# Kernel optimization log

Measured on AMD Instinct MI355X. Metric: run time of the kernel, lower is better.

The kernel has to match this reference:

```python
import jax, jax.numpy as jnp
import numpy as np

N_POINTS = 8192
N_DIM = 2
N_PAIRS = 262144


def setup_inputs() -> dict:
    key = jax.random.key(0)
    k1, k2, k3, k4 = jax.random.split(key, 4)
    logits = jax.random.normal(k1, (N_POINTS, N_DIM), dtype=jnp.float32)
    i = jax.random.randint(k2, (N_PAIRS,), 0, N_POINTS, dtype=jnp.int64)
    j = jax.random.randint(k3, (N_PAIRS,), 0, N_POINTS, dtype=jnp.int64)
    pij = jax.random.uniform(k4, (N_PAIRS,), dtype=jnp.float32, minval=1e-6, maxval=1.0)
    pij = pij / jnp.sum(pij)  # joint probabilities, strictly positive
    return {"pij": pij, "i": i, "j": j, "logits": logits}


def reference(pij, i, j, logits):
    # Pairwise squared distances via the norm expansion (same math as the
    # N x N x D expanded-subtract in the torch original, without the huge tensor).
    sq = jnp.sum(logits * logits, axis=1)                      # [N]
    dkl2 = sq[:, None] + sq[None, :] - 2.0 * (logits @ logits.T)  # [N, N]
    n_diag = logits.shape[0]
    # Student-t partition function, excluding the diagonal (each diag term is 1).
    part = jnp.sum(1.0 / (1.0 + dkl2)) - n_diag
    xi = logits[i]                                              # [E, D]
    xj = logits[j]                                              # [E, D]
    # NOTE: torch adds 1.0 elementwise BEFORE summing over D, so this is
    # (D + ||xi-xj||^2)^-1 — reproduced faithfully.
    num = 1.0 / jnp.sum(1.0 + (xi - xj) ** 2, axis=1)           # [E]
    qij = num / part
    return jnp.sum(pij * (jnp.log(pij) - jnp.log(qij)))
```

## Files before the change

### kernel.cpp

```cpp
#include <hip/hip_runtime.h>
#include <math.h>

#define N_POINTS 8192
#define N_PAIRS  262144

constexpr int BLOCKS  = 512;
constexpr int THREADS = 256;
constexpr int ROWS    = N_POINTS / BLOCKS;
constexpr int TPR     = THREADS / ROWS;
constexpr int EPB     = N_PAIRS / BLOCKS;

__global__ __launch_bounds__(THREADS)
void fused_kernel(const float* __restrict__ logits,
                  const float* __restrict__ pij,
                  const int* __restrict__ ei,
                  const int* __restrict__ ej,
                  float* __restrict__ partials) {
    __shared__ float2 pts[N_POINTS];
    __shared__ float wred[3][THREADS / 64];

    const int t = threadIdx.x;
    const int b = blockIdx.x;

    {
        const float4* src = (const float4*)logits;
        float4* dst = (float4*)pts;
        #pragma unroll
        for (int k = t; k < N_POINTS / 2; k += THREADS) dst[k] = src[k];
    }
    __syncthreads();

    const int row = b * ROWS + (t / TPR);
    const int c0  = t % TPR;
    const float px = pts[row].x;
    const float py = pts[row].y;

    float a0 = 0.f, a1 = 0.f, a2 = 0.f, a3 = 0.f;
    #pragma unroll 2
    for (int k = c0; k < N_POINTS; k += 4 * TPR) {
        const float2 p0 = pts[k];
        const float2 p1 = pts[k + TPR];
        const float2 p2 = pts[k + 2 * TPR];
        const float2 p3 = pts[k + 3 * TPR];
        float dx, dy, d2;
        dx = px - p0.x; dy = py - p0.y;
        d2 = __builtin_fmaf(dx, dx, __builtin_fmaf(dy, dy, 1.0f));
        a0 += __builtin_amdgcn_rcpf(d2);
        dx = px - p1.x; dy = py - p1.y;
        d2 = __builtin_fmaf(dx, dx, __builtin_fmaf(dy, dy, 1.0f));
        a1 += __builtin_amdgcn_rcpf(d2);
        dx = px - p2.x; dy = py - p2.y;
        d2 = __builtin_fmaf(dx, dx, __builtin_fmaf(dy, dy, 1.0f));
        a2 += __builtin_amdgcn_rcpf(d2);
        dx = px - p3.x; dy = py - p3.y;
        d2 = __builtin_fmaf(dx, dx, __builtin_fmaf(dy, dy, 1.0f));
        a3 += __builtin_amdgcn_rcpf(d2);
    }
    float part = (a0 + a1) + (a2 + a3);

    float s1 = 0.f, sp = 0.f;
    #pragma unroll
    for (int it = 0; it < EPB / THREADS; ++it) {
        const int e = b * EPB + it * THREADS + t;
        const int ia = ei[e];
        const int ib = ej[e];
        const float2 pa = pts[ia];
        const float2 pb = pts[ib];
        const float dx = pa.x - pb.x;
        const float dy = pa.y - pb.y;
        const float d2 = __builtin_fmaf(dx, dx, __builtin_fmaf(dy, dy, 2.0f));
        const float p  = pij[e];
        s1 += p * (__logf(p) + __logf(d2));
        sp += p;
    }

    #pragma unroll
    for (int off = 32; off > 0; off >>= 1) {
        part += __shfl_down(part, off, 64);
        s1   += __shfl_down(s1,   off, 64);
        sp   += __shfl_down(sp,   off, 64);
    }
    const int w = t >> 6, l = t & 63;
    if (l == 0) { wred[0][w] = part; wred[1][w] = s1; wred[2][w] = sp; }
    __syncthreads();
    if (t == 0) {
        float r0 = 0.f, r1 = 0.f, r2 = 0.f;
        #pragma unroll
        for (int i = 0; i < THREADS / 64; ++i) {
            r0 += wred[0][i]; r1 += wred[1][i]; r2 += wred[2][i];
        }
        partials[0 * BLOCKS + b] = r0;
        partials[1 * BLOCKS + b] = r1;
        partials[2 * BLOCKS + b] = r2;
    }
}

__global__ __launch_bounds__(256)
void final_kernel(const float* __restrict__ partials, float* __restrict__ out) {
    __shared__ double ra[4], rs[4], rp[4];
    const int t = threadIdx.x;

    double a = (double)partials[0 * BLOCKS + t] + (double)partials[0 * BLOCKS + t + 256];
    double s = (double)partials[1 * BLOCKS + t] + (double)partials[1 * BLOCKS + t + 256];
    double p = (double)partials[2 * BLOCKS + t] + (double)partials[2 * BLOCKS + t + 256];

    #pragma unroll
    for (int off = 32; off > 0; off >>= 1) {
        a += __shfl_down(a, off, 64);
        s += __shfl_down(s, off, 64);
        p += __shfl_down(p, off, 64);
    }
    const int w = t >> 6, l = t & 63;
    if (l == 0) { ra[w] = a; rs[w] = s; rp[w] = p; }
    __syncthreads();
    if (t == 0) {
        double A = 0.0, S = 0.0, P = 0.0;
        #pragma unroll
        for (int i = 0; i < 4; ++i) { A += ra[i]; S += rs[i]; P += rp[i]; }
        A -= (double)N_POINTS;
        out[0] = (float)(S + log(A) * P);
    }
}

extern "C" void kernel_launch(void* const* d_in, const int* in_sizes, int n_in,
                              void* d_out, int out_size, void* d_ws, size_t ws_size,
                              hipStream_t stream) {
    const float* pij    = (const float*)d_in[0];
    const int*   ei     = (const int*)d_in[1];
    const int*   ej     = (const int*)d_in[2];
    const float* logits = (const float*)d_in[3];
    float* out = (float*)d_out;

    float* partials = (float*)d_ws;

    fused_kernel<<<BLOCKS, THREADS, 0, stream>>>(logits, pij, ei, ej, partials);
    final_kernel<<<1, 256, 0, stream>>>(partials, out);
}
```

Measured before the change: 81.49 us.

## Exploit symmetry of pairwise kernel to halve partition-function work

Computes only the upper triangle of the Student-t pair sum, pairing row g with row N-1-g per thread group to balance triangular work, then doubles the total instead of subtracting the diagonal. This is meant to cut the O(N^2) reciprocal work roughly in half. In exchange it drops the manual 4-way unrolled accumulators, adds loop-bound variability, and slightly changes the floating-point summation order.

```diff
diff --git a/kernel.cpp b/kernel.cpp
--- a/kernel.cpp
+++ b/kernel.cpp
@@ -6,8 +6,8 @@
 
 constexpr int BLOCKS  = 512;
 constexpr int THREADS = 256;
-constexpr int ROWS    = N_POINTS / BLOCKS;
-constexpr int TPR     = THREADS / ROWS;
+constexpr int VROWS   = (N_POINTS / 2) / BLOCKS;
+constexpr int TPV     = THREADS / VROWS;
 constexpr int EPB     = N_PAIRS / BLOCKS;
 
 __global__ __launch_bounds__(THREADS)
@@ -30,35 +30,36 @@
     }
     __syncthreads();
 
-    const int row = b * ROWS + (t / TPR);
-    const int c0  = t % TPR;
-    const float px = pts[row].x;
-    const float py = pts[row].y;
+    const int g  = b * VROWS + (t / TPV);
+    const int c0 = t % TPV;
+    const int i_row = g;
+    const int j_row = N_POINTS - 1 - g;
 
-    float a0 = 0.f, a1 = 0.f, a2 = 0.f, a3 = 0.f;
-    #pragma unroll 2
-    for (int k = c0; k < N_POINTS; k += 4 * TPR) {
-        const float2 p0 = pts[k];
-        const float2 p1 = pts[k + TPR];
-        const float2 p2 = pts[k + 2 * TPR];
-        const float2 p3 = pts[k + 3 * TPR];
-        float dx, dy, d2;
-        dx = px - p0.x; dy = py - p0.y;
-        d2 = __builtin_fmaf(dx, dx, __builtin_fmaf(dy, dy, 1.0f));
-        a0 += __builtin_amdgcn_rcpf(d2);
-        dx = px - p1.x; dy = py - p1.y;
-        d2 = __builtin_fmaf(dx, dx, __builtin_fmaf(dy, dy, 1.0f));
-        a1 += __builtin_amdgcn_rcpf(d2);
-        dx = px - p2.x; dy = py - p2.y;
-        d2 = __builtin_fmaf(dx, dx, __builtin_fmaf(dy, dy, 1.0f));
-        a2 += __builtin_amdgcn_rcpf(d2);
-        dx = px - p3.x; dy = py - p3.y;
-        d2 = __builtin_fmaf(dx, dx, __builtin_fmaf(dy, dy, 1.0f));
-        a3 += __builtin_amdgcn_rcpf(d2);
+    float acc1 = 0.0f, acc2 = 0.0f;
+
+    {
+        const float px = pts[i_row].x, py = pts[i_row].y;
+        for (int k = i_row + 1 + c0; k < N_POINTS; k += TPV) {
+            const float2 q = pts[k];
+            const float dx = px - q.x;
+            const float dy = py - q.y;
+            const float d2 = __builtin_fmaf(dx, dx, __builtin_fmaf(dy, dy, 1.0f));
+            acc1 += __builtin_amdgcn_rcpf(d2);
+        }
     }
-    float part = (a0 + a1) + (a2 + a3);
+    {
+        const float px = pts[j_row].x, py = pts[j_row].y;
+        for (int k = j_row + 1 + c0; k < N_POINTS; k += TPV) {
+            const float2 q = pts[k];
+            const float dx = px - q.x;
+            const float dy = py - q.y;
+            const float d2 = __builtin_fmaf(dx, dx, __builtin_fmaf(dy, dy, 1.0f));
+            acc2 += __builtin_amdgcn_rcpf(d2);
+        }
+    }
+    float part = acc1 + acc2;
 
-    float s1 = 0.f, sp = 0.f;
+    float s1 = 0.0f, sp = 0.0f;
     #pragma unroll
     for (int it = 0; it < EPB / THREADS; ++it) {
         const int e = b * EPB + it * THREADS + t;
@@ -117,7 +118,7 @@
         double A = 0.0, S = 0.0, P = 0.0;
         #pragma unroll
         for (int i = 0; i < 4; ++i) { A += ra[i]; S += rs[i]; P += rp[i]; }
-        A -= (double)N_POINTS;
+        A *= 2.0;
         out[0] = (float)(S + log(A) * P);
     }
 }
```

Result: no change. 80.52 us (-1.2%).
